# Kernel tuning notes

Hardware: AMD Instinct MI355X
Metric: run time of the kernel (lower is better)

The kernel has to match this reference:

```python
import jax, jax.numpy as jnp
import numpy as np

# Fixed hierarchical grouping of the 15 regions into 5 groups of 3 (from split_regions)
SPLIT_IDX = np.array([[0, 1, 8], [2, 4, 6], [3, 5, 7], [9, 11, 13], [10, 12, 14]])
BN_EPS = 1e-5


def _bn_relu(x, g, b):
    # BatchNorm over (batch, spatial) dims in training-stats mode, then ReLU
    mu = jnp.mean(x, axis=(0, 2, 3), keepdims=True)
    var = jnp.var(x, axis=(0, 2, 3), keepdims=True)
    xn = (x - mu) * jax.lax.rsqrt(var + BN_EPS)
    return jax.nn.relu(xn * g[None, :, None, None] + b[None, :, None, None])


def _local_agg(x, params):
    # x: [B, Cin, G, K]; pointwise conv (1x1) -> BN -> ReLU per layer, then max over K
    for W, g, b in params:
        x = jnp.einsum('oi,bigk->bogk', W, x)
        x = _bn_relu(x, g, b)
    return jnp.max(x, axis=-1)  # [B, Cout, G]


def setup_inputs() -> dict:
    key = jax.random.key(0)
    ks = jax.random.split(key, 8)
    B, G, K = 32, 15, 2048
    inp = {"local_regions": jax.random.normal(ks[0], (B, G, K, 3), jnp.float32)}
    chans = [(3, 64, 64), (67, 128, 128), (131, 256, 256)]
    ki = 1
    for li, (c0, c1, c2) in enumerate(chans):
        for wi, (co, ci) in enumerate([(c1, c0), (c2, c1)]):
            inp[f"la{li}_w{wi}"] = jax.random.normal(ks[ki], (co, ci), jnp.float32) * (1.0 / np.sqrt(ci))
            inp[f"la{li}_g{wi}"] = jnp.ones((co,), jnp.float32)
            inp[f"la{li}_b{wi}"] = jnp.zeros((co,), jnp.float32)
            ki += 1
    return inp


def reference(local_regions,
              la0_w0, la0_g0, la0_b0, la0_w1, la0_g1, la0_b1,
              la1_w0, la1_g0, la1_b0, la1_w1, la1_g1, la1_b1,
              la2_w0, la2_g0, la2_b0, la2_w1, la2_g1, la2_b1):
    la0 = [(la0_w0, la0_g0, la0_b0), (la0_w1, la0_g1, la0_b1)]
    la1 = [(la1_w0, la1_g0, la1_b0), (la1_w1, la1_g1, la1_b1)]
    la2 = [(la2_w0, la2_g0, la2_b0), (la2_w1, la2_g1, la2_b1)]
    idx = jnp.asarray(SPLIT_IDX)

    x = jnp.transpose(local_regions, (0, 3, 1, 2))  # [B, 3, 15, K]
    centroids_1 = jnp.mean(x, axis=-1)              # [B, 3, 15]
    relative_1 = x - centroids_1[..., None]
    lf1 = _local_agg(relative_1, la0)               # [B, 64, 15]
    local_features = jnp.concatenate([centroids_1, lf1], axis=1)  # [B, 67, 15]

    # level 2: regroup 15 regions into [5, 3]
    lf1_s = jnp.transpose(lf1, (0, 2, 1))[:, idx, :]         # [B, 5, 3, 64]
    lr2 = jnp.transpose(centroids_1, (0, 2, 1))[:, idx, :]   # [B, 5, 3, 3]
    c2 = jnp.mean(lr2, axis=2)                               # [B, 5, 3]
    rel2 = lr2 - c2[:, :, None, :]
    feats2 = jnp.concatenate([rel2, lf1_s], axis=-1)         # [B, 5, 3, 67]
    feats2 = jnp.transpose(feats2, (0, 3, 1, 2))             # [B, 67, 5, 3]
    lf2 = _local_agg(feats2, la1)                            # [B, 128, 5]

    # level 3: global
    c3 = jnp.mean(c2, axis=1)                                # [B, 3]
    rel3 = c2 - c3[:, None, :]                               # [B, 5, 3]
    lf2 = jnp.concatenate([jnp.transpose(rel3, (0, 2, 1)), lf2], axis=1)  # [B, 131, 5]
    lf2 = lf2[:, :, None, :]                                 # [B, 131, 1, 5]
    gf = _local_agg(lf2, la2)                                # [B, 256, 1]
    return gf.squeeze(2), local_features
```

## Files before the change

### kernel.cpp

```cpp
#include <hip/hip_runtime.h>
#include <math.h>

#define GG 15
#define KK 2048
#define NB 480
#define N1F 983040.0f
#define EPS 1e-5f
#define PZN ((int)0xAAAAAAAA)

typedef _Float16 half8 __attribute__((ext_vector_type(8)));
typedef float f32x4 __attribute__((ext_vector_type(4)));

#define CENT  0
#define GSREL 1920
#define GBN1  2160
#define SELO  6256
#define FBN1  36976
#define P2A   37104
#define P2B   45296
#define P3A   53488
#define P3B   69872
#define CA0   86256
#define CA1   86272
#define CD1   86288
#define CT2   86304
#define CT3   86320
#define CT4   86336
#define CT5   86352

#define SMEMF 7936

__device__ const int SIDX[15] = {0,1,8, 2,4,6, 3,5,7, 9,11,13, 10,12,14};

__device__ __forceinline__ float wave_sum(float v){
    for (int off = 32; off; off >>= 1) v += __shfl_down(v, off, 64);
    return v;
}
__device__ __forceinline__ float aloadf(const float* p){
    return __hip_atomic_load(p, __ATOMIC_RELAXED, __HIP_MEMORY_SCOPE_AGENT);
}
__device__ __forceinline__ int aloadi(const int* p){
    return __hip_atomic_load(p, __ATOMIC_RELAXED, __HIP_MEMORY_SCOPE_AGENT);
}
template<int SLP>
__device__ __forceinline__ void fbar(int* c, int target){
    __syncthreads();
    if (threadIdx.x == 0) {
        atomicAdd(c, 1);
        int g = 0;
        while (aloadi(c) != target && ++g < 8000000)
            __builtin_amdgcn_s_sleep(SLP);
    }
    __syncthreads();
    asm volatile("" ::: "memory");
}

__global__ void __launch_bounds__(256, 2) mega(
        const float* __restrict__ x,
        const float* __restrict__ w00, const float* __restrict__ g00, const float* __restrict__ b00,
        const float* __restrict__ w01, const float* __restrict__ g01, const float* __restrict__ b01,
        const float* __restrict__ w10, const float* __restrict__ g10, const float* __restrict__ b10,
        const float* __restrict__ w11, const float* __restrict__ g11, const float* __restrict__ b11,
        const float* __restrict__ w20, const float* __restrict__ g20, const float* __restrict__ b20,
        const float* __restrict__ w21, const float* __restrict__ g21, const float* __restrict__ b21,
        float* __restrict__ ws, float* __restrict__ out) {
    __shared__ __align__(16) float smemf[SMEMF];
    float* xls  = smemf;
    float* redM = smemf + 6144; float* redN = smemf + 6400;
    float* redS = smemf + 6656; float* redQ = smemf + 6912;
    float* bcast= smemf + 7168;
    float* s1ls  = smemf;
    float* t1ls  = smemf + 64;
    float* centb = smemf + 128;
    float* c2b   = smemf + 176;
    float* c3b   = smemf + 192;
    float* f2b   = smemf + 256;
    float* vb    = smemf + 1344;
    float* f3b   = smemf + 3392;
    float* u3b   = smemf + 4052;
    float* c2s   = smemf + 5332;
    float* c2t   = smemf + 5460;
    int* wsi = (int*)ws;

    int bid = blockIdx.x, tid = threadIdx.x;
    int b_ = bid / GG, g_ = bid % GG;
    int wv = tid >> 6, lane = tid & 63, l15 = lane & 15, quad = lane >> 4;
    int gi = bid >> 4;

    {
        const float4* xp4 = (const float4*)(x + (size_t)bid * KK * 3);
        float4* xls4 = (float4*)xls;
        #pragma unroll
        for (int i = 0; i < 6; i++) xls4[i*256 + tid] = xp4[i*256 + tid];
        __syncthreads();
        float m[9] = {0,0,0,0,0,0,0,0,0};
        float a[24];
        const float* bp = &xls[tid*24];
        #pragma unroll
        for (int i = 0; i < 6; i++)
            *reinterpret_cast<float4*>(&a[i*4]) = *reinterpret_cast<const float4*>(&bp[i*4]);
        #pragma unroll
        for (int p = 0; p < 8; p++) {
            float ax=a[p*3], ay=a[p*3+1], az=a[p*3+2];
            m[0]+=ax; m[1]+=ay; m[2]+=az;
            m[3]=fmaf(ax,ax,m[3]); m[4]=fmaf(ay,ay,m[4]); m[5]=fmaf(az,az,m[5]);
            m[6]=fmaf(ax,ay,m[6]); m[7]=fmaf(ax,az,m[7]); m[8]=fmaf(ay,az,m[8]);
        }
        #pragma unroll
        for (int q = 0; q < 9; q++) {
            float v = wave_sum(m[q]);
            if (lane == 0) redM[q*4 + wv] = v;
        }
        __syncthreads();
        if (tid == 0) {
            float t[9];
            #pragma unroll
            for (int q = 0; q < 9; q++) t[q] = redM[q*4]+redM[q*4+1]+redM[q*4+2]+redM[q*4+3];
            float c0 = t[0]/KK, c1 = t[1]/KK, c2 = t[2]/KK;
            bcast[0]=c0; bcast[1]=c1; bcast[2]=c2;
            out[8192 + b_*(67*GG) + 0*GG + g_] = c0;
            out[8192 + b_*(67*GG) + 1*GG + g_] = c1;
            out[8192 + b_*(67*GG) + 2*GG + g_] = c2;
            atomicExch(&ws[CENT + bid*4 + 0], c0);
            atomicExch(&ws[CENT + bid*4 + 1], c1);
            atomicExch(&ws[CENT + bid*4 + 2], c2);
            redM[40] = t[3] - KK*c0*c0;  redM[41] = t[4] - KK*c1*c1;
            redM[42] = t[5] - KK*c2*c2;  redM[43] = t[6] - KK*c0*c1;
            redM[44] = t[7] - KK*c0*c2;  redM[45] = t[8] - KK*c1*c2;
        }
        __syncthreads();
    }
    if (tid < 6) atomicAdd(&ws[GSREL + gi*8 + tid], redM[40 + tid]);

    half8 afA[4], afB[4];
    #pragma unroll
    for (int t = 0; t < 4; t++)
        #pragma unroll
        for (int j = 0; j < 8; j++) {
            afA[t][j] = (_Float16)w01[(t*16 + l15)*64 + quad*8 + j];
            afB[t][j] = (_Float16)w01[(t*16 + l15)*64 + 32 + quad*8 + j];
        }

    fbar<4>(&wsi[CA0], PZN + 480);

    if (tid < 6) {
        float acc = 0.f;
        #pragma unroll
        for (int s = 0; s < 30; s++) acc += aloadf(&ws[GSREL + s*8 + tid]);
        bcast[3+tid] = acc / N1F;
    }
    __syncthreads();
    float c0 = bcast[0], c1 = bcast[1], c2v = bcast[2];
    float S00=bcast[3], S11=bcast[4], S22=bcast[5], S01=bcast[6], S02=bcast[7], S12=bcast[8];

    float wa0[8], wa1[8], wa2[8], ba[8], wb0[8], wb1[8], wb2[8], bb[8];
    #pragma unroll
    for (int j = 0; j < 8; j++) {
        int cA = quad*8 + j;
        float u0=w00[cA*3+0], u1=w00[cA*3+1], u2=w00[cA*3+2];
        float var = u0*u0*S00 + u1*u1*S11 + u2*u2*S22
                  + 2.f*(u0*u1*S01 + u0*u2*S02 + u1*u2*S12);
        float a1 = g00[cA]*rsqrtf(var + EPS);
        wa0[j]=a1*u0; wa1[j]=a1*u1; wa2[j]=a1*u2; ba[j]=b00[cA];
        int cB = cA + 32;
        float v0=w00[cB*3+0], v1=w00[cB*3+1], v2=w00[cB*3+2];
        float varB = v0*v0*S00 + v1*v1*S11 + v2*v2*S22
                   + 2.f*(v0*v1*S01 + v0*v2*S02 + v1*v2*S12);
        float a1B = g00[cB]*rsqrtf(varB + EPS);
        wb0[j]=a1B*v0; wb1[j]=a1B*v1; wb2[j]=a1B*v2; bb[j]=b00[cB];
    }
    float mx[16], mn[16], sm[16], sq[16];
    #pragma unroll
    for (int s = 0; s < 16; s++) { mx[s]=-1e30f; mn[s]=1e30f; sm[s]=0.f; sq[s]=0.f; }

    for (int it = 0; it < 32; it++) {
        int k = it*64 + wv*16 + l15;
        float r0 = xls[k*3+0]-c0, r1 = xls[k*3+1]-c1, r2 = xls[k*3+2]-c2v;
        half8 bf0, bf1;
        #pragma unroll
        for (int j = 0; j < 8; j++) {
            float pA = fmaf(wa0[j],r0, fmaf(wa1[j],r1, fmaf(wa2[j],r2, ba[j])));
            bf0[j] = (_Float16)fmaxf(pA, 0.f);
            float pB = fmaf(wb0[j],r0, fmaf(wb1[j],r1, fmaf(wb2[j],r2, bb[j])));
            bf1[j] = (_Float16)fmaxf(pB, 0.f);
        }
        #pragma unroll
        for (int t = 0; t < 4; t++) {
            f32x4 acc = {0.f,0.f,0.f,0.f};
            acc = __builtin_amdgcn_mfma_f32_16x16x32_f16(afA[t], bf0, acc, 0, 0, 0);
            acc = __builtin_amdgcn_mfma_f32_16x16x32_f16(afB[t], bf1, acc, 0, 0, 0);
            #pragma unroll
            for (int r = 0; r < 4; r++) {
                float h = acc[r];
                int s = t*4 + r;
                mx[s]=fmaxf(mx[s],h); mn[s]=fminf(mn[s],h);
                sm[s]+=h;             sq[s]=fmaf(h,h,sq[s]);
            }
        }
    }
    #pragma unroll
    for (int m = 1; m < 16; m <<= 1) {
        #pragma unroll
        for (int s = 0; s < 16; s++) {
            mx[s] = fmaxf(mx[s], __shfl_xor(mx[s], m, 64));
            mn[s] = fminf(mn[s], __shfl_xor(mn[s], m, 64));
            sm[s] += __shfl_xor(sm[s], m, 64);
            sq[s] += __shfl_xor(sq[s], m, 64);
        }
    }
    __syncthreads();
    if (l15 == 0) {
        #pragma unroll
        for (int t = 0; t < 4; t++)
            #pragma unroll
            for (int r = 0; r < 4; r++) {
                int o = t*16 + quad*4 + r;
                redM[wv*64+o]=mx[t*4+r]; redN[wv*64+o]=mn[t*4+r];
                redS[wv*64+o]=sm[t*4+r]; redQ[wv*64+o]=sq[t*4+r];
            }
    }
    __syncthreads();
    float Mreg = -1e30f, Nreg = 1e30f;
    if (tid < 64) {
        float S=0.f, Q=0.f;
        #pragma unroll
        for (int w = 0; w < 4; w++) {
            Mreg = fmaxf(Mreg, redM[w*64+tid]); Nreg = fminf(Nreg, redN[w*64+tid]);
            S += redS[w*64+tid];               Q += redQ[w*64+tid];
        }
        atomicAdd(&ws[GBN1 + b_*128 + tid], S);
        atomicAdd(&ws[GBN1 + b_*128 + 64 + tid], Q);
        float sel = (g01[tid] >= 0.f) ? Mreg : Nreg;
        atomicExch(&ws[SELO + bid*64 + tid], sel);
    }

    __syncthreads();
    if (tid == 0) atomicAdd(&wsi[CA1], 1);
    if (bid == 0) {
        if (tid == 0) {
            int g = 0;
            while (aloadi(&wsi[CA1]) != PZN + 480 && ++g < 8000000)
                __builtin_amdgcn_s_sleep(2);
        }
        __syncthreads();
        if (tid < 128) {
            float acc = 0.f;
            #pragma unroll
            for (int i = 0; i < 32; i++) acc += aloadf(&ws[GBN1 + i*128 + tid]);
            atomicExch(&ws[FBN1 + tid], acc);
        }
        __syncthreads();
        if (tid == 0) atomicAdd(&wsi[CD1], 1);
    }
    if (tid == 0) {
        int g = 0;
        while (aloadi(&wsi[CD1]) != PZN + 1 && ++g < 8000000)
            __builtin_amdgcn_s_sleep(2);
    }
    __syncthreads();
    asm volatile("" ::: "memory");

    if (tid < 64) {
        float S = aloadf(&ws[FBN1 + tid]);
        float Q = aloadf(&ws[FBN1 + 64 + tid]);
        float mean = S / N1F;
        float var  = Q / N1F - mean*mean;
        float s1 = g01[tid]*rsqrtf(var + EPS);
        float t1 = b01[tid] - mean*s1;
        float val = fmaxf(fmaf(s1, (s1 >= 0.f) ? Mreg : Nreg, t1), 0.f);
        out[8192 + b_*(67*GG) + (3+tid)*GG + g_] = val;
        s1ls[tid] = s1; t1ls[tid] = t1;
    }
    if (g_ != 0) return;

    int half_ = tid >> 7, oc = tid & 127, pbase = half_*8, npts = 8 - half_;
    float acc1[8], acc2[8], a3[5], a3b[5];

    {
        if (tid < 45) centb[tid] = aloadf(&ws[CENT + (b_*GG + tid/3)*4 + tid%3]);
        if (tid >= 188) f2b[15*68 + (tid - 188)] = 0.f;
        __syncthreads();
        if (tid < 15) {
            int s = tid/3, i = tid%3;
            c2b[tid] = (centb[SIDX[s*3+0]*3+i] + centb[SIDX[s*3+1]*3+i]
                      + centb[SIDX[s*3+2]*3+i]) * (1.f/3.f);
        }
        __syncthreads();
        if (tid < 3)
            c3b[tid] = (c2b[tid]+c2b[3+tid]+c2b[6+tid]+c2b[9+tid]+c2b[12+tid]) * 0.2f;
        if (tid < 45) {
            int p = tid/3, i = tid%3;
            f2b[p*68 + i] = centb[SIDX[p]*3+i] - c2b[(p/3)*3 + i];
        }
        for (int u = tid; u < 960; u += 256) {
            int p = u >> 6, ch = u & 63, src = b_*GG + SIDX[p];
            float sel = aloadf(&ws[SELO + src*64 + ch]);
            f2b[p*68 + 3 + ch] = fmaxf(fmaf(s1ls[ch], sel, t1ls[ch]), 0.f);
        }
        __syncthreads();
        #pragma unroll
        for (int q = 0; q < 8; q++) acc1[q] = 0.f;
        const float* wr = w10 + oc*67;
        #pragma unroll 4
        for (int c = 0; c < 67; c++) {
            float wv_ = wr[c];
            #pragma unroll
            for (int q = 0; q < 8; q++)
                acc1[q] = fmaf(wv_, f2b[(pbase+q)*68 + c], acc1[q]);
        }
        float S = 0.f, Q = 0.f;
        #pragma unroll
        for (int q = 0; q < 8; q++) if (q < npts) { S += acc1[q]; Q = fmaf(acc1[q],acc1[q],Q); }
        redS[tid] = S; redQ[tid] = Q;
        __syncthreads();
        if (tid < 128) {
            atomicExch(&ws[P2A + b_*256 + tid],       redS[tid] + redS[128 + tid]);
            atomicExch(&ws[P2A + b_*256 + 128 + tid], redQ[tid] + redQ[128 + tid]);
        }
    }
    fbar<1>(&wsi[CT2], PZN + 32);

    {
        if (tid < 128) {
            float S = 0.f, Q = 0.f;
            #pragma unroll
            for (int i = 0; i < 32; i++) {
                S += aloadf(&ws[P2A + i*256 + tid]);
                Q += aloadf(&ws[P2A + i*256 + 128 + tid]);
            }
            float mean = S / 480.f, var = Q / 480.f - mean*mean;
            float s2 = g10[tid]*rsqrtf(var + EPS);
            c2s[tid] = s2; c2t[tid] = b10[tid] - mean*s2;
            vb[15*128 + tid] = 0.f;
        }
        __syncthreads();
        {
            float s2 = c2s[oc], t2 = c2t[oc];
            #pragma unroll
            for (int q = 0; q < 8; q++) {
                float v = fmaxf(fmaf(s2, acc1[q], t2), 0.f);
                if (q < npts) vb[(pbase+q)*128 + oc] = v;
            }
        }
        __syncthreads();
        #pragma unroll
        for (int q = 0; q < 8; q++) acc2[q] = 0.f;
        const float4* w4 = (const float4*)(w11 + oc*128);
        #pragma unroll 2
        for (int c4 = 0; c4 < 32; c4++) {
            float4 wv4 = w4[c4];
            int cb = c4*4;
            #pragma unroll
            for (int q = 0; q < 8; q++) {
                const float* vrow = &vb[(pbase+q)*128];
                acc2[q] = fmaf(wv4.x, vrow[cb+0], acc2[q]);
                acc2[q] = fmaf(wv4.y, vrow[cb+1], acc2[q]);
                acc2[q] = fmaf(wv4.z, vrow[cb+2], acc2[q]);
                acc2[q] = fmaf(wv4.w, vrow[cb+3], acc2[q]);
            }
        }
        float S = 0.f, Q = 0.f;
        #pragma unroll
        for (int q = 0; q < 8; q++) if (q < npts) { S += acc2[q]; Q = fmaf(acc2[q],acc2[q],Q); }
        redS[tid] = S; redQ[tid] = Q;
        __syncthreads();
        if (tid < 128) {
            atomicExch(&ws[P2B + b_*256 + tid],       redS[tid] + redS[128 + tid]);
            atomicExch(&ws[P2B + b_*256 + 128 + tid], redQ[tid] + redQ[128 + tid]);
        }
    }
    fbar<1>(&wsi[CT3], PZN + 32);

    {
        if (tid < 128) {
            float S = 0.f, Q = 0.f;
            #pragma unroll
            for (int i = 0; i < 32; i++) {
                S += aloadf(&ws[P2B + i*256 + tid]);
                Q += aloadf(&ws[P2B + i*256 + 128 + tid]);
            }
            float mean = S / 480.f, var = Q / 480.f - mean*mean;
            float s3 = g11[tid]*rsqrtf(var + EPS);
            c2s[tid] = s3; c2t[tid] = b11[tid] - mean*s3;
        }
        __syncthreads();
        {
            float s3 = c2s[oc], t3 = c2t[oc];
            #pragma unroll
            for (int q = 0; q < 8; q++) {
                float v = fmaxf(fmaf(s3, acc2[q], t3), 0.f);
                if (q < npts) vb[(pbase+q)*128 + oc] = v;
            }
        }
        __syncthreads();
        for (int u = tid; u < 640; u += 256) {
            int s = u >> 7, ch = u & 127;
            f3b[s*132 + 3 + ch] = fmaxf(fmaxf(vb[(3*s)*128+ch], vb[(3*s+1)*128+ch]),
                                        vb[(3*s+2)*128+ch]);
        }
        if (tid < 15) {
            int s = tid/3, i = tid%3;
            f3b[s*132 + i] = c2b[tid] - c3b[i];
        }
        __syncthreads();
        #pragma unroll
        for (int s = 0; s < 5; s++) a3[s] = 0.f;
        const float* wr = w20 + tid*131;
        #pragma unroll 4
        for (int c = 0; c < 131; c++) {
            float wv_ = wr[c];
            #pragma unroll
            for (int s = 0; s < 5; s++)
                a3[s] = fmaf(wv_, f3b[s*132 + c], a3[s]);
        }
        float S = 0.f, Q = 0.f;
        #pragma unroll
        for (int s = 0; s < 5; s++) { S += a3[s]; Q = fmaf(a3[s],a3[s],Q); }
        atomicExch(&ws[P3A + b_*512 + tid], S);
        atomicExch(&ws[P3A + b_*512 + 256 + tid], Q);
    }
    fbar<1>(&wsi[CT4], PZN + 32);

    {
        {
            float S = 0.f, Q = 0.f;
            #pragma unroll
            for (int i = 0; i < 32; i++) {
                S += aloadf(&ws[P3A + i*512 + tid]);
                Q += aloadf(&ws[P3A + i*512 + 256 + tid]);
            }
            float mean = S / 160.f, var = Q / 160.f - mean*mean;
            float s4 = g20[tid]*rsqrtf(var + EPS);
            float t4 = b20[tid] - mean*s4;
            #pragma unroll
            for (int s = 0; s < 5; s++)
                u3b[s*256 + tid] = fmaxf(fmaf(s4, a3[s], t4), 0.f);
        }
        __syncthreads();
        #pragma unroll
        for (int s = 0; s < 5; s++) a3b[s] = 0.f;
        const float4* w4 = (const float4*)(w21 + tid*256);
        #pragma unroll 2
        for (int c4 = 0; c4 < 64; c4++) {
            float4 wv4 = w4[c4];
            int cb = c4*4;
            #pragma unroll
            for (int s = 0; s < 5; s++) {
                const float* ur = &u3b[s*256];
                a3b[s] = fmaf(wv4.x, ur[cb+0], a3b[s]);
                a3b[s] = fmaf(wv4.y, ur[cb+1], a3b[s]);
                a3b[s] = fmaf(wv4.z, ur[cb+2], a3b[s]);
                a3b[s] = fmaf(wv4.w, ur[cb+3], a3b[s]);
            }
        }
        float S = 0.f, Q = 0.f;
        #pragma unroll
        for (int s = 0; s < 5; s++) { S += a3b[s]; Q = fmaf(a3b[s],a3b[s],Q); }
        atomicExch(&ws[P3B + b_*512 + tid], S);
        atomicExch(&ws[P3B + b_*512 + 256 + tid], Q);
    }
    fbar<1>(&wsi[CT5], PZN + 32);

    {
        float S = 0.f, Q = 0.f;
        #pragma unroll
        for (int i = 0; i < 32; i++) {
            S += aloadf(&ws[P3B + i*512 + tid]);
            Q += aloadf(&ws[P3B + i*512 + 256 + tid]);
        }
        float mean = S / 160.f, var = Q / 160.f - mean*mean;
        float s5 = g21[tid]*rsqrtf(var + EPS);
        float t5 = b21[tid] - mean*s5;
        float m = -1e30f;
        #pragma unroll
        for (int s = 0; s < 5; s++)
            m = fmaxf(m, fmaxf(fmaf(s5, a3b[s], t5), 0.f));
        out[b_*256 + tid] = m;
    }
}

extern "C" void kernel_launch(void* const* d_in, const int* in_sizes, int n_in,
                              void* d_out, int out_size, void* d_ws, size_t ws_size,
                              hipStream_t stream) {
    (void)in_sizes; (void)n_in; (void)out_size; (void)ws_size;
    const float* x   = (const float*)d_in[0];
    const float* w00 = (const float*)d_in[1];
    const float* g00 = (const float*)d_in[2];
    const float* b00 = (const float*)d_in[3];
    const float* w01 = (const float*)d_in[4];
    const float* g01 = (const float*)d_in[5];
    const float* b01 = (const float*)d_in[6];
    const float* w10 = (const float*)d_in[7];
    const float* g10 = (const float*)d_in[8];
    const float* b10 = (const float*)d_in[9];
    const float* w11 = (const float*)d_in[10];
    const float* g11 = (const float*)d_in[11];
    const float* b11 = (const float*)d_in[12];
    const float* w20 = (const float*)d_in[13];
    const float* g20 = (const float*)d_in[14];
    const float* b20 = (const float*)d_in[15];
    const float* w21 = (const float*)d_in[16];
    const float* g21 = (const float*)d_in[17];
    const float* b21 = (const float*)d_in[18];
    float* out = (float*)d_out;
    float* ws  = (float*)d_ws;

    mega<<<NB, 256, 0, stream>>>(x, w00,g00,b00, w01,g01,b01, w10,g10,b10,
                                 w11,g11,b11, w20,g20,b20, w21,g21,b21, ws, out);
}
```

Before: 203.8 us.

## Spread level-2/3 layers across all blocks and use hierarchical grid barriers

Instead of letting only the 32 g_==0 blocks compute the level-2 and level-3 pointwise layers, every one of the 480 blocks now computes a slice of output channels (9 rows for level 2, 18 for level 3). Each block writes its pre-activations to workspace and accumulates BN statistics with atomics into two super-group partials. The flat global counter barriers are replaced by a two-level barrier: group counters feed a super counter, and the last arriver runs an optional fold and sets per-group flags. The aim is to cut the serial tail run by few blocks and to reduce atomic contention on one counter. The cost is more global round trips through workspace and more barriers executed by all blocks.

```diff
diff --git a/kernel.cpp b/kernel.cpp
--- a/kernel.cpp
+++ b/kernel.cpp
@@ -16,17 +16,17 @@
 #define GBN1  2160
 #define SELO  6256
 #define FBN1  36976
-#define P2A   37104
-#define P2B   45296
-#define P3A   53488
-#define P3B   69872
-#define CA0   86256
-#define CA1   86272
-#define CD1   86288
-#define CT2   86304
-#define CT3   86320
-#define CT4   86336
-#define CT5   86352
+#define H2A   37104
+#define H2B   98544
+#define H3A   159984
+#define H3B   200944
+#define GS2A  241904
+#define GS2B  242416
+#define GS3A  242928
+#define GS3B  243952
+#define CGRP  244976
+#define CSUP  247856
+#define CFLG  247952
 
 #define SMEMF 7936
 
@@ -42,18 +42,33 @@
 __device__ __forceinline__ int aloadi(const int* p){
     return __hip_atomic_load(p, __ATOMIC_RELAXED, __HIP_MEMORY_SCOPE_AGENT);
 }
-template<int SLP>
-__device__ __forceinline__ void fbar(int* c, int target){
-    __syncthreads();
+template<int SLP, class Fold>
+__device__ __forceinline__ void gbar2(int* wsi, int idx, int gi, int* sflag,
+                                      Fold fold){
+    __syncthreads();
+    if (threadIdx.x == 0)
+        sflag[0] = (atomicAdd(&wsi[CGRP + (idx*30 + gi)*16], 1) == PZN + 15) ? 1 : 0;
+    __syncthreads();
+    if (sflag[0]) {
+        if (threadIdx.x == 0)
+            sflag[1] = (atomicAdd(&wsi[CSUP + idx*16], 1) == PZN + 29) ? 1 : 0;
+        __syncthreads();
+        if (sflag[1]) {
+            fold();
+            __syncthreads();
+            if (threadIdx.x < 30)
+                atomicExch(&wsi[CFLG + (idx*30 + threadIdx.x)*16], 1);
+        }
+    }
     if (threadIdx.x == 0) {
-        atomicAdd(c, 1);
         int g = 0;
-        while (aloadi(c) != target && ++g < 8000000)
+        while (aloadi(&wsi[CFLG + (idx*30 + gi)*16]) != 1 && ++g < 8000000)
             __builtin_amdgcn_s_sleep(SLP);
     }
     __syncthreads();
     asm volatile("" ::: "memory");
 }
+struct NoFold { __device__ void operator()() const {} };
 
 __global__ void __launch_bounds__(256, 2) mega(
         const float* __restrict__ x,
@@ -69,23 +84,30 @@
     float* redM = smemf + 6144; float* redN = smemf + 6400;
     float* redS = smemf + 6656; float* redQ = smemf + 6912;
     float* bcast= smemf + 7168;
+    int*   sflag= (int*)(smemf + 7916);
     float* s1ls  = smemf;
     float* t1ls  = smemf + 64;
     float* centb = smemf + 128;
     float* c2b   = smemf + 176;
     float* c3b   = smemf + 192;
     float* f2b   = smemf + 256;
-    float* vb    = smemf + 1344;
+    float* vls   = smemf + 1344;
     float* f3b   = smemf + 3392;
     float* u3b   = smemf + 4052;
     float* c2s   = smemf + 5332;
     float* c2t   = smemf + 5460;
+    float* s4ls  = smemf + 5588;
+    float* t4ls  = smemf + 5844;
+    float* hst   = redS;
     int* wsi = (int*)ws;
 
     int bid = blockIdx.x, tid = threadIdx.x;
     int b_ = bid / GG, g_ = bid % GG;
     int wv = tid >> 6, lane = tid & 63, l15 = lane & 15, quad = lane >> 4;
     int gi = bid >> 4;
+    int sgrp = b_ >> 4;
+    int base2 = g_*9,  nr2 = (g_ == 14) ? 2 : 9;
+    int base3 = g_*18, nr3 = (g_ == 14) ? 4 : 18;
 
     {
         const float4* xp4 = (const float4*)(x + (size_t)bid * KK * 3);
@@ -141,7 +163,7 @@
             afB[t][j] = (_Float16)w01[(t*16 + l15)*64 + 32 + quad*8 + j];
         }
 
-    fbar<4>(&wsi[CA0], PZN + 480);
+    gbar2<4>(wsi, 0, gi, sflag, NoFold{});
 
     if (tid < 6) {
         float acc = 0.f;
@@ -234,31 +256,14 @@
         atomicExch(&ws[SELO + bid*64 + tid], sel);
     }
 
-    __syncthreads();
-    if (tid == 0) atomicAdd(&wsi[CA1], 1);
-    if (bid == 0) {
-        if (tid == 0) {
-            int g = 0;
-            while (aloadi(&wsi[CA1]) != PZN + 480 && ++g < 8000000)
-                __builtin_amdgcn_s_sleep(2);
-        }
-        __syncthreads();
+    gbar2<4>(wsi, 1, gi, sflag, [&]{
         if (tid < 128) {
             float acc = 0.f;
             #pragma unroll
             for (int i = 0; i < 32; i++) acc += aloadf(&ws[GBN1 + i*128 + tid]);
             atomicExch(&ws[FBN1 + tid], acc);
         }
-        __syncthreads();
-        if (tid == 0) atomicAdd(&wsi[CD1], 1);
-    }
-    if (tid == 0) {
-        int g = 0;
-        while (aloadi(&wsi[CD1]) != PZN + 1 && ++g < 8000000)
-            __builtin_amdgcn_s_sleep(2);
-    }
-    __syncthreads();
-    asm volatile("" ::: "memory");
+    });
 
     if (tid < 64) {
         float S = aloadf(&ws[FBN1 + tid]);
@@ -271,210 +276,173 @@
         out[8192 + b_*(67*GG) + (3+tid)*GG + g_] = val;
         s1ls[tid] = s1; t1ls[tid] = t1;
     }
-    if (g_ != 0) return;
-
-    int half_ = tid >> 7, oc = tid & 127, pbase = half_*8, npts = 8 - half_;
-    float acc1[8], acc2[8], a3[5], a3b[5];
+
+    if (tid < 45) centb[tid] = aloadf(&ws[CENT + (b_*GG + tid/3)*4 + tid%3]);
+    __syncthreads();
+    if (tid < 15) {
+        int s = tid/3, i = tid%3;
+        c2b[tid] = (centb[SIDX[s*3+0]*3+i] + centb[SIDX[s*3+1]*3+i]
+                  + centb[SIDX[s*3+2]*3+i]) * (1.f/3.f);
+    }
+    __syncthreads();
+    if (tid < 3)
+        c3b[tid] = (c2b[tid]+c2b[3+tid]+c2b[6+tid]+c2b[9+tid]+c2b[12+tid]) * 0.2f;
+    if (tid < 45) {
+        int p = tid/3, i = tid%3;
+        f2b[p*68 + i] = centb[SIDX[p]*3+i] - c2b[(p/3)*3 + i];
+    }
+    for (int u = tid; u < 960; u += 256) {
+        int p = u >> 6, ch = u & 63, src = b_*GG + SIDX[p];
+        float sel = aloadf(&ws[SELO + src*64 + ch]);
+        f2b[p*68 + 3 + ch] = fmaxf(fmaf(s1ls[ch], sel, t1ls[ch]), 0.f);
+    }
+    __syncthreads();
+    if (tid < nr2*15) {
+        int rl = tid/15, p = tid%15, r = base2 + rl;
+        const float* wr = w10 + r*67;
+        float h = 0.f;
+        #pragma unroll 4
+        for (int c = 0; c < 67; c++) h = fmaf(wr[c], f2b[p*68 + c], h);
+        atomicExch(&ws[H2A + (b_*GG + p)*128 + r], h);
+        hst[rl*15 + p] = h;
+    }
+    __syncthreads();
+    if (tid < nr2) {
+        int r = base2 + tid;
+        float S = 0.f, Q = 0.f;
+        #pragma unroll
+        for (int p = 0; p < 15; p++) { float v = hst[tid*15+p]; S += v; Q = fmaf(v,v,Q); }
+        atomicAdd(&ws[GS2A + sgrp*256 + r], S);
+        atomicAdd(&ws[GS2A + sgrp*256 + 128 + r], Q);
+    }
+    gbar2<1>(wsi, 2, gi, sflag, NoFold{});
+
+    if (tid < 128) {
+        float S = aloadf(&ws[GS2A + tid])       + aloadf(&ws[GS2A + 256 + tid]);
+        float Q = aloadf(&ws[GS2A + 128 + tid]) + aloadf(&ws[GS2A + 256 + 128 + tid]);
+        float mean = S / 480.f, var = Q / 480.f - mean*mean;
+        float s2 = g10[tid]*rsqrtf(var + EPS);
+        c2s[tid] = s2; c2t[tid] = b10[tid] - mean*s2;
+    }
+    __syncthreads();
+    for (int u = tid; u < 1920; u += 256) {
+        int p = u >> 7, ch = u & 127;
+        float hv = aloadf(&ws[H2A + (b_*GG + p)*128 + ch]);
+        vls[p*128 + ch] = fmaxf(fmaf(c2s[ch], hv, c2t[ch]), 0.f);
+    }
+    __syncthreads();
+    if (tid < nr2*15) {
+        int rl = tid/15, p = tid%15, r = base2 + rl;
+        const float* wr = w11 + r*128;
+        const float* vp = &vls[p*128];
+        float h = 0.f;
+        #pragma unroll 4
+        for (int c = 0; c < 128; c++) h = fmaf(wr[c], vp[c], h);
+        atomicExch(&ws[H2B + (b_*GG + p)*128 + r], h);
+        hst[rl*15 + p] = h;
+    }
+    __syncthreads();
+    if (tid < nr2) {
+        int r = base2 + tid;
+        float S = 0.f, Q = 0.f;
+        #pragma unroll
+        for (int p = 0; p < 15; p++) { float v = hst[tid*15+p]; S += v; Q = fmaf(v,v,Q); }
+        atomicAdd(&ws[GS2B + sgrp*256 + r], S);
+        atomicAdd(&ws[GS2B + sgrp*256 + 128 + r], Q);
+    }
+    gbar2<1>(wsi, 3, gi, sflag, NoFold{});
+
+    if (tid < 128) {
+        float S = aloadf(&ws[GS2B + tid])       + aloadf(&ws[GS2B + 256 + tid]);
+        float Q = aloadf(&ws[GS2B + 128 + tid]) + aloadf(&ws[GS2B + 256 + 128 + tid]);
+        float mean = S / 480.f, var = Q / 480.f - mean*mean;
+        float s3 = g11[tid]*rsqrtf(var + EPS);
+        c2s[tid] = s3; c2t[tid] = b11[tid] - mean*s3;
+    }
+    __syncthreads();
+    for (int u = tid; u < 640; u += 256) {
+        int s = u >> 7, ch = u & 127;
+        float sv = c2s[ch], tv = c2t[ch], m = -1e30f;
+        #pragma unroll
+        for (int j = 0; j < 3; j++) {
+            float hv = aloadf(&ws[H2B + (b_*GG + 3*s + j)*128 + ch]);
+            m = fmaxf(m, fmaxf(fmaf(sv, hv, tv), 0.f));
+        }
+        f3b[s*132 + 3 + ch] = m;
+    }
+    if (tid < 15) {
+        int s = tid/3, i = tid%3;
+        f3b[s*132 + i] = c2b[tid] - c3b[i];
+    }
+    __syncthreads();
+    if (tid < nr3*5) {
+        int rl = tid/5, s = tid%5, r = base3 + rl;
+        const float* wr = w20 + r*131;
+        const float* fp = &f3b[s*132];
+        float h = 0.f;
+        #pragma unroll 4
+        for (int c = 0; c < 131; c++) h = fmaf(wr[c], fp[c], h);
+        atomicExch(&ws[H3A + (b_*5 + s)*256 + r], h);
+        hst[rl*5 + s] = h;
+    }
+    __syncthreads();
+    if (tid < nr3) {
+        int r = base3 + tid;
+        float S = 0.f, Q = 0.f;
+        #pragma unroll
+        for (int s = 0; s < 5; s++) { float v = hst[tid*5+s]; S += v; Q = fmaf(v,v,Q); }
+        atomicAdd(&ws[GS3A + sgrp*512 + r], S);
+        atomicAdd(&ws[GS3A + sgrp*512 + 256 + r], Q);
+    }
+    gbar2<1>(wsi, 4, gi, sflag, NoFold{});
 
     {
-        if (tid < 45) centb[tid] = aloadf(&ws[CENT + (b_*GG + tid/3)*4 + tid%3]);
-        if (tid >= 188) f2b[15*68 + (tid - 188)] = 0.f;
-        __syncthreads();
-        if (tid < 15) {
-            int s = tid/3, i = tid%3;
-            c2b[tid] = (centb[SIDX[s*3+0]*3+i] + centb[SIDX[s*3+1]*3+i]
-                      + centb[SIDX[s*3+2]*3+i]) * (1.f/3.f);
-        }
-        __syncthreads();
-        if (tid < 3)
-            c3b[tid] = (c2b[tid]+c2b[3+tid]+c2b[6+tid]+c2b[9+tid]+c2b[12+tid]) * 0.2f;
-        if (tid < 45) {
-            int p = tid/3, i = tid%3;
-            f2b[p*68 + i] = centb[SIDX[p]*3+i] - c2b[(p/3)*3 + i];
-        }
-        for (int u = tid; u < 960; u += 256) {
-            int p = u >> 6, ch = u & 63, src = b_*GG + SIDX[p];
-            float sel = aloadf(&ws[SELO + src*64 + ch]);
-            f2b[p*68 + 3 + ch] = fmaxf(fmaf(s1ls[ch], sel, t1ls[ch]), 0.f);
-        }
-        __syncthreads();
-        #pragma unroll
-        for (int q = 0; q < 8; q++) acc1[q] = 0.f;
-        const float* wr = w10 + oc*67;
+        float S = aloadf(&ws[GS3A + tid])       + aloadf(&ws[GS3A + 512 + tid]);
+        float Q = aloadf(&ws[GS3A + 256 + tid]) + aloadf(&ws[GS3A + 512 + 256 + tid]);
+        float mean = S / 160.f, var = Q / 160.f - mean*mean;
+        float s4 = g20[tid]*rsqrtf(var + EPS);
+        s4ls[tid] = s4; t4ls[tid] = b20[tid] - mean*s4;
+    }
+    __syncthreads();
+    for (int u = tid; u < 1280; u += 256) {
+        int s = u >> 8, ch = u & 255;
+        float hv = aloadf(&ws[H3A + (b_*5 + s)*256 + ch]);
+        u3b[s*256 + ch] = fmaxf(fmaf(s4ls[ch], hv, t4ls[ch]), 0.f);
+    }
+    __syncthreads();
+    if (tid < nr3*5) {
+        int rl = tid/5, s = tid%5, r = base3 + rl;
+        const float* wr = w21 + r*256;
+        const float* up = &u3b[s*256];
+        float h = 0.f;
         #pragma unroll 4
-        for (int c = 0; c < 67; c++) {
-            float wv_ = wr[c];
-            #pragma unroll
-            for (int q = 0; q < 8; q++)
-                acc1[q] = fmaf(wv_, f2b[(pbase+q)*68 + c], acc1[q]);
-        }
+        for (int c = 0; c < 256; c++) h = fmaf(wr[c], up[c], h);
+        atomicExch(&ws[H3B + (b_*5 + s)*256 + r], h);
+        hst[rl*5 + s] = h;
+    }
+    __syncthreads();
+    if (tid < nr3) {
+        int r = base3 + tid;
         float S = 0.f, Q = 0.f;
         #pragma unroll
-        for (int q = 0; q < 8; q++) if (q < npts) { S += acc1[q]; Q = fmaf(acc1[q],acc1[q],Q); }
-        redS[tid] = S; redQ[tid] = Q;
-        __syncthreads();
-        if (tid < 128) {
-            atomicExch(&ws[P2A + b_*256 + tid],       redS[tid] + redS[128 + tid]);
-            atomicExch(&ws[P2A + b_*256 + 128 + tid], redQ[tid] + redQ[128 + tid]);
-        }
-    }
-    fbar<1>(&wsi[CT2], PZN + 32);
-
-    {
-        if (tid < 128) {
-            float S = 0.f, Q = 0.f;
-            #pragma unroll
-            for (int i = 0; i < 32; i++) {
-                S += aloadf(&ws[P2A + i*256 + tid]);
-                Q += aloadf(&ws[P2A + i*256 + 128 + tid]);
-            }
-            float mean = S / 480.f, var = Q / 480.f - mean*mean;
-            float s2 = g10[tid]*rsqrtf(var + EPS);
-            c2s[tid] = s2; c2t[tid] = b10[tid] - mean*s2;
-            vb[15*128 + tid] = 0.f;
-        }
-        __syncthreads();
-        {
-            float s2 = c2s[oc], t2 = c2t[oc];
-            #pragma unroll
-            for (int q = 0; q < 8; q++) {
-                float v = fmaxf(fmaf(s2, acc1[q], t2), 0.f);
-                if (q < npts) vb[(pbase+q)*128 + oc] = v;
-            }
-        }
-        __syncthreads();
-        #pragma unroll
-        for (int q = 0; q < 8; q++) acc2[q] = 0.f;
-        const float4* w4 = (const float4*)(w11 + oc*128);
-        #pragma unroll 2
-        for (int c4 = 0; c4 < 32; c4++) {
-            float4 wv4 = w4[c4];
-            int cb = c4*4;
-            #pragma unroll
-            for (int q = 0; q < 8; q++) {
-                const float* vrow = &vb[(pbase+q)*128];
-                acc2[q] = fmaf(wv4.x, vrow[cb+0], acc2[q]);
-                acc2[q] = fmaf(wv4.y, vrow[cb+1], acc2[q]);
-                acc2[q] = fmaf(wv4.z, vrow[cb+2], acc2[q]);
-                acc2[q] = fmaf(wv4.w, vrow[cb+3], acc2[q]);
-            }
-        }
-        float S = 0.f, Q = 0.f;
-        #pragma unroll
-        for (int q = 0; q < 8; q++) if (q < npts) { S += acc2[q]; Q = fmaf(acc2[q],acc2[q],Q); }
-        redS[tid] = S; redQ[tid] = Q;
-        __syncthreads();
-        if (tid < 128) {
-            atomicExch(&ws[P2B + b_*256 + tid],       redS[tid] + redS[128 + tid]);
-            atomicExch(&ws[P2B + b_*256 + 128 + tid], redQ[tid] + redQ[128 + tid]);
-        }
-    }
-    fbar<1>(&wsi[CT3], PZN + 32);
-
-    {
-        if (tid < 128) {
-            float S = 0.f, Q = 0.f;
-            #pragma unroll
-            for (int i = 0; i < 32; i++) {
-                S += aloadf(&ws[P2B + i*256 + tid]);
-                Q += aloadf(&ws[P2B + i*256 + 128 + tid]);
-            }
-            float mean = S / 480.f, var = Q / 480.f - mean*mean;
-            float s3 = g11[tid]*rsqrtf(var + EPS);
-            c2s[tid] = s3; c2t[tid] = b11[tid] - mean*s3;
-        }
-        __syncthreads();
-        {
-            float s3 = c2s[oc], t3 = c2t[oc];
-            #pragma unroll
-            for (int q = 0; q < 8; q++) {
-                float v = fmaxf(fmaf(s3, acc2[q], t3), 0.f);
-                if (q < npts) vb[(pbase+q)*128 + oc] = v;
-            }
-        }
-        __syncthreads();
-        for (int u = tid; u < 640; u += 256) {
-            int s = u >> 7, ch = u & 127;
-            f3b[s*132 + 3 + ch] = fmaxf(fmaxf(vb[(3*s)*128+ch], vb[(3*s+1)*128+ch]),
-                                        vb[(3*s+2)*128+ch]);
-        }
-        if (tid < 15) {
-            int s = tid/3, i = tid%3;
-            f3b[s*132 + i] = c2b[tid] - c3b[i];
-        }
-        __syncthreads();
-        #pragma unroll
-        for (int s = 0; s < 5; s++) a3[s] = 0.f;
-        const float* wr = w20 + tid*131;
-        #pragma unroll 4
-        for (int c = 0; c < 131; c++) {
-            float wv_ = wr[c];
-            #pragma unroll
-            for (int s = 0; s < 5; s++)
-                a3[s] = fmaf(wv_, f3b[s*132 + c], a3[s]);
-        }
-        float S = 0.f, Q = 0.f;
-        #pragma unroll
-        for (int s = 0; s < 5; s++) { S += a3[s]; Q = fmaf(a3[s],a3[s],Q); }
-        atomicExch(&ws[P3A + b_*512 + tid], S);
-        atomicExch(&ws[P3A + b_*512 + 256 + tid], Q);
-    }
-    fbar<1>(&wsi[CT4], PZN + 32);
-
-    {
-        {
-            float S = 0.f, Q = 0.f;
-            #pragma unroll
-            for (int i = 0; i < 32; i++) {
-                S += aloadf(&ws[P3A + i*512 + tid]);
-                Q += aloadf(&ws[P3A + i*512 + 256 + tid]);
-            }
-            float mean = S / 160.f, var = Q / 160.f - mean*mean;
-            float s4 = g20[tid]*rsqrtf(var + EPS);
-            float t4 = b20[tid] - mean*s4;
-            #pragma unroll
-            for (int s = 0; s < 5; s++)
-                u3b[s*256 + tid] = fmaxf(fmaf(s4, a3[s], t4), 0.f);
-        }
-        __syncthreads();
-        #pragma unroll
-        for (int s = 0; s < 5; s++) a3b[s] = 0.f;
-        const float4* w4 = (const float4*)(w21 + tid*256);
-        #pragma unroll 2
-        for (int c4 = 0; c4 < 64; c4++) {
-            float4 wv4 = w4[c4];
-            int cb = c4*4;
-            #pragma unroll
-            for (int s = 0; s < 5; s++) {
-                const float* ur = &u3b[s*256];
-                a3b[s] = fmaf(wv4.x, ur[cb+0], a3b[s]);
-                a3b[s] = fmaf(wv4.y, ur[cb+1], a3b[s]);
-                a3b[s] = fmaf(wv4.z, ur[cb+2], a3b[s]);
-                a3b[s] = fmaf(wv4.w, ur[cb+3], a3b[s]);
-            }
-        }
-        float S = 0.f, Q = 0.f;
-        #pragma unroll
-        for (int s = 0; s < 5; s++) { S += a3b[s]; Q = fmaf(a3b[s],a3b[s],Q); }
-        atomicExch(&ws[P3B + b_*512 + tid], S);
-        atomicExch(&ws[P3B + b_*512 + 256 + tid], Q);
-    }
-    fbar<1>(&wsi[CT5], PZN + 32);
-
-    {
-        float S = 0.f, Q = 0.f;
-        #pragma unroll
-        for (int i = 0; i < 32; i++) {
-            S += aloadf(&ws[P3B + i*512 + tid]);
-            Q += aloadf(&ws[P3B + i*512 + 256 + tid]);
-        }
+        for (int s = 0; s < 5; s++) { float v = hst[tid*5+s]; S += v; Q = fmaf(v,v,Q); }
+        atomicAdd(&ws[GS3B + sgrp*512 + r], S);
+        atomicAdd(&ws[GS3B + sgrp*512 + 256 + r], Q);
+    }
+    gbar2<1>(wsi, 5, gi, sflag, NoFold{});
+
+    if (g_ == 0) {
+        float S = aloadf(&ws[GS3B + tid])       + aloadf(&ws[GS3B + 512 + tid]);
+        float Q = aloadf(&ws[GS3B + 256 + tid]) + aloadf(&ws[GS3B + 512 + 256 + tid]);
         float mean = S / 160.f, var = Q / 160.f - mean*mean;
         float s5 = g21[tid]*rsqrtf(var + EPS);
         float t5 = b21[tid] - mean*s5;
         float m = -1e30f;
         #pragma unroll
-        for (int s = 0; s < 5; s++)
-            m = fmaxf(m, fmaxf(fmaf(s5, a3b[s], t5), 0.f));
+        for (int s = 0; s < 5; s++) {
+            float hv = aloadf(&ws[H3B + (b_*5 + s)*256 + tid]);
+            m = fmaxf(m, fmaxf(fmaf(s5, hv, t5), 0.f));
+        }
         out[b_*256 + tid] = m;
     }
 }
```

Result: faster. 180.7 us (-11.3%).
